# Optimization experiments

Measured on AMD Instinct MI355X. Metric: run time of the kernel, lower is better.

## Reference

```python
import jax, jax.numpy as jnp
import numpy as np

N_TOKENS = 4096
EMBED = 2048
D_ATTN = 2048


def setup_inputs() -> dict:
    key = jax.random.key(0)
    k1, k2, k3, k4 = jax.random.split(key, 4)
    # torch.rand -> uniform [0,1); keeps scores positive so the multiplicative
    # -inf mask acts as a clean causal mask (faithful to original behavior).
    token_embeddings = jax.random.uniform(k1, (N_TOKENS, EMBED), dtype=jnp.float32)
    W_Q = jax.random.uniform(k2, (EMBED, D_ATTN), dtype=jnp.float32)
    W_K = jax.random.uniform(k3, (EMBED, D_ATTN), dtype=jnp.float32)
    W_V = jax.random.uniform(k4, (EMBED, D_ATTN), dtype=jnp.float32)
    return {"token_embeddings": token_embeddings, "W_Q": W_Q, "W_K": W_K, "W_V": W_V}


def reference(token_embeddings, W_Q, W_K, W_V):
    n = token_embeddings.shape[0]
    d = W_Q.shape[1]
    # mask: 1 on/below diagonal, -inf strictly above (multiplicative, as in source)
    neg_inf = jnp.float32(-jnp.inf)
    mask = jnp.tril(jnp.ones((n, n), dtype=jnp.float32)) + jnp.triu(
        jnp.full((n, n), neg_inf, dtype=jnp.float32), k=1
    )
    Q = token_embeddings @ W_Q          # (n, d)
    K = token_embeddings @ W_K          # (n, d)
    V = token_embeddings @ W_V          # (n, d)
    scores = (Q @ K.T) * mask           # (n, n); upper tri -> -inf (scores > 0)
    scores = scores / jnp.sqrt(jnp.float32(d))
    attn = jax.nn.softmax(scores, axis=-1)
    return attn @ V                     # (n, d)
```

## Files before the change

### kernel.cpp

```cpp
#include <hip/hip_runtime.h>
#include <hip/hip_bf16.h>
#include <cstdint>
#include <cstddef>

#define N_TOK 4096
#define EMB   2048
#define DATT  2048

typedef __attribute__((ext_vector_type(8))) short short8;
typedef __attribute__((ext_vector_type(4))) short shortx4;
typedef __attribute__((ext_vector_type(4))) float f32x4;

#define MFMA(a, b, c) __builtin_amdgcn_mfma_f32_16x16x32_bf16(a, b, c, 0, 0, 0)

__device__ __forceinline__ short f2bs(float f) {
  __hip_bfloat16 h = __float2bfloat16(f);
  return __builtin_bit_cast(short, h);
}
__device__ __forceinline__ float bs2f(short s) {
  return __uint_as_float(((unsigned)(unsigned short)s) << 16);
}
__device__ __forceinline__ float ldin(const void* p, size_t i, int isbf) {
  if (isbf) {
    unsigned short u = ((const unsigned short*)p)[i];
    return __uint_as_float(((unsigned int)u) << 16);
  }
  return ((const float*)p)[i];
}

__device__ __forceinline__ size_t swz(int r, int c, int kdim) {
  return ((size_t)((r >> 7) * (kdim >> 3) + (c >> 3)) << 10) +
         (size_t)((r & 127) << 3) + (c & 7);
}

__global__ void k_sniff(const void* x, int* flag) {
  if (threadIdx.x == 0 && blockIdx.x == 0) {
    const unsigned short* u = (const unsigned short*)x;
    int bf = 1;
    for (int i = 0; i < 256; ++i) {
      unsigned short v = u[i];
      if ((v & 0x8000u) || ((v & 0x7FFFu) >= 0x3F80u)) { bf = 0; break; }
    }
    *flag = bf;
  }
}

__global__ __launch_bounds__(256) void k_xbar(const void* X, float* xbar,
                                              const int* flagp) {
  int isbf = *flagp;
  int e = blockIdx.x * 256 + threadIdx.x;
  float s = 0.f;
  for (int r = 0; r < 256; ++r) s += ldin(X, (size_t)r * EMB + e, isbf);
  xbar[e] = s * (1.f / 256.f);
}

__global__ __launch_bounds__(256) void k_split_x(const void* X, short* Xh, short* Xl,
                                                 const int* flagp) {
  int isbf = *flagp;
  size_t base = ((size_t)blockIdx.x * 256 + threadIdx.x) * 4;
  int r = (int)(base >> 11), c = (int)(base & 2047);
  shortx4 h, l;
#pragma unroll
  for (int u = 0; u < 4; ++u) {
    float x = ldin(X, base + u, isbf);
    short hh = f2bs(x);
    h[u] = hh;
    l[u] = f2bs(x - bs2f(hh));
  }
  size_t o = swz(r, c, EMB);
  *(shortx4*)(Xh + o) = h;
  *(shortx4*)(Xl + o) = l;
}

__global__ __launch_bounds__(256) void k_transpose_split(const void* W, short* Wth,
                                                         short* Wtl, int R, int C,
                                                         const int* flagp, int wlo) {
  __shared__ float T[64][65];
  int isbf = *flagp;
  int r0 = blockIdx.y * 64, c0 = blockIdx.x * 64;
  int tid = threadIdx.x;
#pragma unroll
  for (int it = 0; it < 16; ++it) {
    int idx = tid + it * 256;
    int row = idx >> 6, col = idx & 63;
    T[row][col] = ldin(W, (size_t)(r0 + row) * C + c0 + col, isbf);
  }
  __syncthreads();
#pragma unroll
  for (int it = 0; it < 16; ++it) {
    int idx = tid + it * 256;
    int row = idx >> 6, col = idx & 63;
    float x = T[col][row];
    short h = f2bs(x);
    size_t o = swz(c0 + row, r0 + col, R);
    Wth[o] = h;
    if (wlo) Wtl[o] = f2bs(x - bs2f(h));
  }
}

__global__ __launch_bounds__(256) void k_kbar(const short* Wth, const short* Wtl,
                                              const float* xbar, float* kbar) {
  int d = blockIdx.x;
  float s = 0.f;
  for (int e = threadIdx.x; e < EMB; e += 256) {
    size_t o = swz(d, e, EMB);
    s += xbar[e] * (bs2f(Wth[o]) + bs2f(Wtl[o]));
  }
  __shared__ float red[4];
#pragma unroll
  for (int off = 32; off > 0; off >>= 1) s += __shfl_down(s, off);
  if ((threadIdx.x & 63) == 0) red[threadIdx.x >> 6] = s;
  __syncthreads();
  if (threadIdx.x == 0) kbar[d] = red[0] + red[1] + red[2] + red[3];
}

__global__ __launch_bounds__(256) void k_proj_d(const short* Ah, const short* Al,
                                                const short* Bh, const short* Bl,
                                                short* Ch, short* Cl,
                                                const float* bias) {
  int tid = threadIdx.x;
  int wave = tid >> 6, lane = tid & 63;
  int ln = lane & 15, quad = lane >> 4;
  int wm = (wave >> 1) * 64, wn = (wave & 1) * 64;
  int row0 = blockIdx.y * 128, col0 = blockIdx.x * 128;
  const short8* A8h = (const short8*)Ah + (size_t)(row0 >> 7) * (256 * 128);
  const short8* A8l = (const short8*)Al + (size_t)(row0 >> 7) * (256 * 128);
  const short8* B8h = (const short8*)Bh + (size_t)(col0 >> 7) * (256 * 128);
  const short8* B8l = (const short8*)Bl + (size_t)(col0 >> 7) * (256 * 128);
  f32x4 acc[4][4] = {};
  for (int k0 = 0; k0 < EMB; k0 += 32) {
    int t = (k0 >> 3) + quad;
    short8 fah[4], fal[4], fbh[4], fbl[4];
#pragma unroll
    for (int i = 0; i < 4; ++i) {
      int ar = wm + i * 16 + ln;
      fah[i] = A8h[t * 128 + ar];
      fal[i] = A8l[t * 128 + ar];
    }
#pragma unroll
    for (int j = 0; j < 4; ++j) {
      int br = wn + j * 16 + ln;
      fbh[j] = B8h[t * 128 + br];
      fbl[j] = B8l[t * 128 + br];
    }
#pragma unroll
    for (int j = 0; j < 4; ++j)
#pragma unroll
      for (int i = 0; i < 4; ++i) {
        acc[i][j] = MFMA(fah[i], fbh[j], acc[i][j]);
        acc[i][j] = MFMA(fah[i], fbl[j], acc[i][j]);
        acc[i][j] = MFMA(fal[i], fbh[j], acc[i][j]);
      }
  }
#pragma unroll
  for (int i = 0; i < 4; ++i)
#pragma unroll
    for (int j = 0; j < 4; ++j)
#pragma unroll
      for (int r = 0; r < 4; ++r) {
        int row = row0 + wm + i * 16 + quad * 4 + r;
        int col = col0 + wn + j * 16 + ln;
        float x = acc[i][j][r];
        if (bias) x -= bias[col];
        short h = f2bs(x);
        size_t o = swz(row, col, DATT);
        Ch[o] = h;
        Cl[o] = f2bs(x - bs2f(h));
      }
}

__global__ __launch_bounds__(256) void k_proj1_d(const short* Ah, const short* Bh,
                                                 short* Ch) {
  int tid = threadIdx.x;
  int wave = tid >> 6, lane = tid & 63;
  int ln = lane & 15, quad = lane >> 4;
  int wm = (wave >> 1) * 64, wn = (wave & 1) * 64;
  int row0 = blockIdx.y * 128, col0 = blockIdx.x * 128;
  const short8* A8h = (const short8*)Ah + (size_t)(row0 >> 7) * (256 * 128);
  const short8* B8h = (const short8*)Bh + (size_t)(col0 >> 7) * (256 * 128);
  f32x4 acc[4][4] = {};
  for (int k0 = 0; k0 < EMB; k0 += 32) {
    int t = (k0 >> 3) + quad;
    short8 fah[4], fbh[4];
#pragma unroll
    for (int i = 0; i < 4; ++i) fah[i] = A8h[t * 128 + wm + i * 16 + ln];
#pragma unroll
    for (int j = 0; j < 4; ++j) fbh[j] = B8h[t * 128 + wn + j * 16 + ln];
#pragma unroll
    for (int j = 0; j < 4; ++j)
#pragma unroll
      for (int i = 0; i < 4; ++i) acc[i][j] = MFMA(fah[i], fbh[j], acc[i][j]);
  }
#pragma unroll
  for (int i = 0; i < 4; ++i)
#pragma unroll
    for (int j = 0; j < 4; ++j)
#pragma unroll
      for (int r = 0; r < 4; ++r) {
        int row = row0 + wm + i * 16 + quad * 4 + r;
        int col = col0 + wn + j * 16 + ln;
        Ch[swz(row, col, N_TOK)] = f2bs(acc[i][j][r]);
      }
}

__global__ __launch_bounds__(256) void k_score_d(const short* Qh, const short* Ql,
                                                 const short* Kh, const short* Kl,
                                                 float* S) {
  if (blockIdx.x > blockIdx.y) return;
  int tid = threadIdx.x;
  int wave = tid >> 6, lane = tid & 63;
  int ln = lane & 15, quad = lane >> 4;
  int wm = (wave >> 1) * 64, wn = (wave & 1) * 64;
  int row0 = blockIdx.y * 128, col0 = blockIdx.x * 128;
  const short8* A8h = (const short8*)Qh + (size_t)(row0 >> 7) * (256 * 128);
  const short8* A8l = (const short8*)Ql + (size_t)(row0 >> 7) * (256 * 128);
  const short8* B8h = (const short8*)Kh + (size_t)(col0 >> 7) * (256 * 128);
  const short8* B8l = (const short8*)Kl + (size_t)(col0 >> 7) * (256 * 128);
  f32x4 acc[4][4] = {};
  for (int k0 = 0; k0 < DATT; k0 += 32) {
    int t = (k0 >> 3) + quad;
    short8 fah[4], fal[4], fbh[4], fbl[4];
#pragma unroll
    for (int i = 0; i < 4; ++i) {
      int ar = wm + i * 16 + ln;
      fah[i] = A8h[t * 128 + ar];
      fal[i] = A8l[t * 128 + ar];
    }
#pragma unroll
    for (int j = 0; j < 4; ++j) {
      int br = wn + j * 16 + ln;
      fbh[j] = B8h[t * 128 + br];
      fbl[j] = B8l[t * 128 + br];
    }
#pragma unroll
    for (int j = 0; j < 4; ++j)
#pragma unroll
      for (int i = 0; i < 4; ++i) {
        acc[i][j] = MFMA(fah[i], fbh[j], acc[i][j]);
        acc[i][j] = MFMA(fah[i], fbl[j], acc[i][j]);
        acc[i][j] = MFMA(fal[i], fbh[j], acc[i][j]);
      }
  }
  const float scale = 0.022097086912079608f;
#pragma unroll
  for (int i = 0; i < 4; ++i)
#pragma unroll
    for (int j = 0; j < 4; ++j)
#pragma unroll
      for (int r = 0; r < 4; ++r) {
        int row = row0 + wm + i * 16 + quad * 4 + r;
        int col = col0 + wn + j * 16 + ln;
        if (col <= row) S[(size_t)row * N_TOK + col] = acc[i][j][r] * scale;
      }
}

__global__ __launch_bounds__(256) void k_softmax(const float* S, short* P) {
  int i = blockIdx.x;
  const float* row = S + (size_t)i * N_TOK;
  int len = i + 1;
  int tid = threadIdx.x;
  __shared__ float red[4];
  float m = -3.402823466e38f;
  for (int j = tid; j < len; j += 256) m = fmaxf(m, row[j]);
#pragma unroll
  for (int off = 32; off > 0; off >>= 1) m = fmaxf(m, __shfl_down(m, off));
  if ((tid & 63) == 0) red[tid >> 6] = m;
  __syncthreads();
  m = fmaxf(fmaxf(red[0], red[1]), fmaxf(red[2], red[3]));
  __syncthreads();
  float s = 0.f;
  for (int j = tid; j < len; j += 256) s += __expf(row[j] - m);
#pragma unroll
  for (int off = 32; off > 0; off >>= 1) s += __shfl_down(s, off);
  if ((tid & 63) == 0) red[tid >> 6] = s;
  __syncthreads();
  s = red[0] + red[1] + red[2] + red[3];
  float inv = 1.f / s;
  size_t rbase = ((size_t)(i >> 7) * (N_TOK >> 3) << 10) + (size_t)((i & 127) << 3);
  for (int j = tid; j < len; j += 256)
    P[rbase + ((size_t)(j >> 3) << 10) + (j & 7)] = f2bs(__expf(row[j] - m) * inv);
  for (int j = len + tid; j < N_TOK; j += 256)
    P[rbase + ((size_t)(j >> 3) << 10) + (j & 7)] = 0;
}

__global__ __launch_bounds__(256) void k_out_d(const short* Ph, const short* Vh,
                                               void* Co, const int* flagp) {
  int isbf = *flagp;
  int tid = threadIdx.x;
  int wave = tid >> 6, lane = tid & 63;
  int ln = lane & 15, quad = lane >> 4;
  int wm = (wave >> 1) * 64, wn = (wave & 1) * 64;
  int row0 = blockIdx.y * 128, col0 = blockIdx.x * 128;
  const short8* A8h = (const short8*)Ph + (size_t)(row0 >> 7) * (512 * 128);
  const short8* B8h = (const short8*)Vh + (size_t)(col0 >> 7) * (512 * 128);
  f32x4 acc[4][4] = {};
  int kmax = row0 + 128;
  for (int k0 = 0; k0 < kmax; k0 += 32) {
    int t = (k0 >> 3) + quad;
    short8 fah[4], fbh[4];
#pragma unroll
    for (int i = 0; i < 4; ++i) fah[i] = A8h[t * 128 + wm + i * 16 + ln];
#pragma unroll
    for (int j = 0; j < 4; ++j) fbh[j] = B8h[t * 128 + wn + j * 16 + ln];
#pragma unroll
    for (int j = 0; j < 4; ++j)
#pragma unroll
      for (int i = 0; i < 4; ++i) acc[i][j] = MFMA(fah[i], fbh[j], acc[i][j]);
  }
#pragma unroll
  for (int i = 0; i < 4; ++i)
#pragma unroll
    for (int j = 0; j < 4; ++j)
#pragma unroll
      for (int r = 0; r < 4; ++r) {
        int row = row0 + wm + i * 16 + quad * 4 + r;
        int col = col0 + wn + j * 16 + ln;
        size_t idx = (size_t)row * DATT + col;
        if (isbf) ((__hip_bfloat16*)Co)[idx] = __float2bfloat16(acc[i][j][r]);
        else      ((float*)Co)[idx] = acc[i][j][r];
      }
}

extern "C" void kernel_launch(void* const* d_in, const int* in_sizes, int n_in,
                              void* d_out, int out_size, void* d_ws, size_t ws_size,
                              hipStream_t stream) {
  const void* X  = d_in[0];
  const void* WQ = d_in[1];
  const void* WK = d_in[2];
  const void* WV = d_in[3];

  float* ws   = (float*)d_ws;
  int*   flag = (int*)d_ws;
  float* xbar = ws + 256;
  float* kbar = ws + 2560;
  short* p0   = (short*)(ws + 16384);
  const size_t M8 = (size_t)N_TOK * DATT;
  const size_t M4 = (size_t)EMB * DATT;
  short* Xh  = p0;
  short* Xl  = Xh + M8;
  short* Wth = Xl + M8;
  short* Wtl = Wth + M4;
  float* S   = (float*)p0;
  short* Qh  = p0 + 4 * M8;
  short* Ql  = Qh + M8;
  short* Kh  = Ql + M8;
  short* Kl  = Kh + M8;
  short* Vt  = Kl + M8;
  short* P   = Qh;

  dim3 blk(256);

  k_sniff<<<1, 64, 0, stream>>>(X, flag);
  k_xbar<<<EMB / 256, blk, 0, stream>>>(X, xbar, flag);
  k_split_x<<<(N_TOK * EMB) / 1024, blk, 0, stream>>>(X, Xh, Xl, flag);

  dim3 gt(DATT / 64, EMB / 64);
  dim3 gq(DATT / 128, N_TOK / 128);
  dim3 gv(N_TOK / 128, DATT / 128);

  k_transpose_split<<<gt, blk, 0, stream>>>(WQ, Wth, Wtl, EMB, DATT, flag, 1);
  k_proj_d<<<gq, blk, 0, stream>>>(Xh, Xl, Wth, Wtl, Qh, Ql, nullptr);
  k_transpose_split<<<gt, blk, 0, stream>>>(WK, Wth, Wtl, EMB, DATT, flag, 1);
  k_kbar<<<DATT, blk, 0, stream>>>(Wth, Wtl, xbar, kbar);
  k_proj_d<<<gq, blk, 0, stream>>>(Xh, Xl, Wth, Wtl, Kh, Kl, kbar);
  k_transpose_split<<<gt, blk, 0, stream>>>(WV, Wth, nullptr, EMB, DATT, flag, 0);
  k_proj1_d<<<gv, blk, 0, stream>>>(Wth, Xh, Vt);

  dim3 gs(N_TOK / 128, N_TOK / 128);
  k_score_d<<<gs, blk, 0, stream>>>(Qh, Ql, Kh, Kl, S);

  k_softmax<<<N_TOK, blk, 0, stream>>>(S, P);

  dim3 go(DATT / 128, N_TOK / 128);
  k_out_d<<<go, blk, 0, stream>>>(P, Vt, d_out, flag);
}
```

Measured before the change: 761.5 us.

## Stage GEMM tiles through double-buffered LDS via direct global-to-LDS loads

Replaces the per-wave direct global loads in all four MFMA GEMM kernels with a shared core that copies each 32-deep K chunk into LDS using global_load_lds, double-buffered so the next chunk loads while the current one is computed. The score kernel now launches only the lower-triangular tiles through a linear index decoded into (row, col) instead of a full grid with early exits. Launch bounds now request two blocks per CU. The intent is to stop each wave fetching operand tiles redundantly from global memory and to hide load latency. The cost is one barrier per K step and up to 64KB of LDS per block in the three-pass variants.

```diff
diff --git a/kernel.cpp b/kernel.cpp
--- a/kernel.cpp
+++ b/kernel.cpp
@@ -2,6 +2,7 @@
 #include <hip/hip_bf16.h>
 #include <cstdint>
 #include <cstddef>
+#include <cmath>
 
 #define N_TOK 4096
 #define EMB   2048
@@ -31,6 +32,83 @@
 __device__ __forceinline__ size_t swz(int r, int c, int kdim) {
   return ((size_t)((r >> 7) * (kdim >> 3) + (c >> 3)) << 10) +
          (size_t)((r & 127) << 3) + (c & 7);
+}
+
+__device__ __forceinline__ void gl16(const short* g, short* l) {
+  __builtin_amdgcn_global_load_lds(
+      (const __attribute__((address_space(1))) unsigned int*)(const void*)g,
+      (__attribute__((address_space(3))) unsigned int*)(void*)l, 16, 0, 0);
+}
+
+template <bool THREE>
+__device__ __forceinline__ void gemm_core(const short* Ah, const short* Al,
+                                          const short* Bh, const short* Bl,
+                                          int chunks, int apan, int bpan,
+                                          int kmax, short* lds,
+                                          f32x4 acc[4][4]) {
+  const int NSL = THREE ? 4 : 2;
+  int tid = threadIdx.x;
+  int lane = tid & 63;
+  int wave = tid >> 6;
+  int ln = lane & 15, quad = lane >> 4;
+  int wm = (wave >> 1) * 64, wn = (wave & 1) * 64;
+  int wofs = wave * 512;
+
+  auto stage = [&](int b, int k0) {
+    size_t ao = ((size_t)(apan * chunks + (k0 >> 3))) << 10;
+    size_t bo = ((size_t)(bpan * chunks + (k0 >> 3))) << 10;
+    short* base = lds + b * NSL * 4096;
+    const short* sa = Ah + ao + tid * 8;
+    const short* sb = Bh + bo + tid * 8;
+    gl16(sa,        base + wofs);
+    gl16(sa + 2048, base + wofs + 2048);
+    gl16(sb,        base + 4096 + wofs);
+    gl16(sb + 2048, base + 4096 + wofs + 2048);
+    if (THREE) {
+      const short* sal = Al + ao + tid * 8;
+      const short* sbl = Bl + bo + tid * 8;
+      gl16(sal,        base + 8192 + wofs);
+      gl16(sal + 2048, base + 8192 + wofs + 2048);
+      gl16(sbl,        base + 12288 + wofs);
+      gl16(sbl + 2048, base + 12288 + wofs + 2048);
+    }
+  };
+
+  stage(0, 0);
+  int cur = 0;
+  int abase = quad * 1024 + (wm + ln) * 8;
+  int bbase = quad * 1024 + (wn + ln) * 8;
+  for (int k0 = 0; k0 < kmax; k0 += 32) {
+    __syncthreads();
+    if (k0 + 32 < kmax) stage(cur ^ 1, k0 + 32);
+    const short* B0 = lds + cur * NSL * 4096;
+    short8 fah[4], fbh[4];
+#pragma unroll
+    for (int i = 0; i < 4; ++i) fah[i] = *(const short8*)(B0 + abase + i * 128);
+#pragma unroll
+    for (int j = 0; j < 4; ++j) fbh[j] = *(const short8*)(B0 + 4096 + bbase + j * 128);
+    if (THREE) {
+      short8 fal[4], fbl[4];
+#pragma unroll
+      for (int i = 0; i < 4; ++i) fal[i] = *(const short8*)(B0 + 8192 + abase + i * 128);
+#pragma unroll
+      for (int j = 0; j < 4; ++j) fbl[j] = *(const short8*)(B0 + 12288 + bbase + j * 128);
+#pragma unroll
+      for (int j = 0; j < 4; ++j)
+#pragma unroll
+        for (int i = 0; i < 4; ++i) {
+          acc[i][j] = MFMA(fah[i], fbh[j], acc[i][j]);
+          acc[i][j] = MFMA(fah[i], fbl[j], acc[i][j]);
+          acc[i][j] = MFMA(fal[i], fbh[j], acc[i][j]);
+        }
+    } else {
+#pragma unroll
+      for (int j = 0; j < 4; ++j)
+#pragma unroll
+        for (int i = 0; i < 4; ++i) acc[i][j] = MFMA(fah[i], fbh[j], acc[i][j]);
+    }
+    cur ^= 1;
+  }
 }
 
 __global__ void k_sniff(const void* x, int* flag) {
@@ -114,44 +192,18 @@
   if (threadIdx.x == 0) kbar[d] = red[0] + red[1] + red[2] + red[3];
 }
 
-__global__ __launch_bounds__(256) void k_proj_d(const short* Ah, const short* Al,
-                                                const short* Bh, const short* Bl,
-                                                short* Ch, short* Cl,
-                                                const float* bias) {
+__global__ __launch_bounds__(256, 2) void k_proj3(const short* Ah, const short* Al,
+                                                  const short* Bh, const short* Bl,
+                                                  short* Ch, short* Cl,
+                                                  const float* bias) {
+  __shared__ short lds[2 * 4 * 4096];
+  f32x4 acc[4][4] = {};
+  int row0 = blockIdx.y * 128, col0 = blockIdx.x * 128;
+  gemm_core<true>(Ah, Al, Bh, Bl, EMB >> 3, row0 >> 7, col0 >> 7, EMB, lds, acc);
   int tid = threadIdx.x;
   int wave = tid >> 6, lane = tid & 63;
   int ln = lane & 15, quad = lane >> 4;
   int wm = (wave >> 1) * 64, wn = (wave & 1) * 64;
-  int row0 = blockIdx.y * 128, col0 = blockIdx.x * 128;
-  const short8* A8h = (const short8*)Ah + (size_t)(row0 >> 7) * (256 * 128);
-  const short8* A8l = (const short8*)Al + (size_t)(row0 >> 7) * (256 * 128);
-  const short8* B8h = (const short8*)Bh + (size_t)(col0 >> 7) * (256 * 128);
-  const short8* B8l = (const short8*)Bl + (size_t)(col0 >> 7) * (256 * 128);
-  f32x4 acc[4][4] = {};
-  for (int k0 = 0; k0 < EMB; k0 += 32) {
-    int t = (k0 >> 3) + quad;
-    short8 fah[4], fal[4], fbh[4], fbl[4];
-#pragma unroll
-    for (int i = 0; i < 4; ++i) {
-      int ar = wm + i * 16 + ln;
-      fah[i] = A8h[t * 128 + ar];
-      fal[i] = A8l[t * 128 + ar];
-    }
-#pragma unroll
-    for (int j = 0; j < 4; ++j) {
-      int br = wn + j * 16 + ln;
-      fbh[j] = B8h[t * 128 + br];
-      fbl[j] = B8l[t * 128 + br];
-    }
-#pragma unroll
-    for (int j = 0; j < 4; ++j)
-#pragma unroll
-      for (int i = 0; i < 4; ++i) {
-        acc[i][j] = MFMA(fah[i], fbh[j], acc[i][j]);
-        acc[i][j] = MFMA(fah[i], fbl[j], acc[i][j]);
-        acc[i][j] = MFMA(fal[i], fbh[j], acc[i][j]);
-      }
-  }
 #pragma unroll
   for (int i = 0; i < 4; ++i)
 #pragma unroll
@@ -169,28 +221,17 @@
       }
 }
 
-__global__ __launch_bounds__(256) void k_proj1_d(const short* Ah, const short* Bh,
-                                                 short* Ch) {
+__global__ __launch_bounds__(256, 2) void k_proj1(const short* Ah, const short* Bh,
+                                                  short* Ch) {
+  __shared__ short lds[2 * 2 * 4096];
+  f32x4 acc[4][4] = {};
+  int row0 = blockIdx.y * 128, col0 = blockIdx.x * 128;
+  gemm_core<false>(Ah, nullptr, Bh, nullptr, EMB >> 3, row0 >> 7, col0 >> 7, EMB,
+                   lds, acc);
   int tid = threadIdx.x;
   int wave = tid >> 6, lane = tid & 63;
   int ln = lane & 15, quad = lane >> 4;
   int wm = (wave >> 1) * 64, wn = (wave & 1) * 64;
-  int row0 = blockIdx.y * 128, col0 = blockIdx.x * 128;
-  const short8* A8h = (const short8*)Ah + (size_t)(row0 >> 7) * (256 * 128);
-  const short8* B8h = (const short8*)Bh + (size_t)(col0 >> 7) * (256 * 128);
-  f32x4 acc[4][4] = {};
-  for (int k0 = 0; k0 < EMB; k0 += 32) {
-    int t = (k0 >> 3) + quad;
-    short8 fah[4], fbh[4];
-#pragma unroll
-    for (int i = 0; i < 4; ++i) fah[i] = A8h[t * 128 + wm + i * 16 + ln];
-#pragma unroll
-    for (int j = 0; j < 4; ++j) fbh[j] = B8h[t * 128 + wn + j * 16 + ln];
-#pragma unroll
-    for (int j = 0; j < 4; ++j)
-#pragma unroll
-      for (int i = 0; i < 4; ++i) acc[i][j] = MFMA(fah[i], fbh[j], acc[i][j]);
-  }
 #pragma unroll
   for (int i = 0; i < 4; ++i)
 #pragma unroll
@@ -203,44 +244,22 @@
       }
 }
 
-__global__ __launch_bounds__(256) void k_score_d(const short* Qh, const short* Ql,
-                                                 const short* Kh, const short* Kl,
-                                                 float* S) {
-  if (blockIdx.x > blockIdx.y) return;
+__global__ __launch_bounds__(256, 2) void k_score3(const short* Qh, const short* Ql,
+                                                   const short* Kh, const short* Kl,
+                                                   float* S) {
+  int bi = blockIdx.x;
+  int by = (int)((sqrtf(8.f * (float)bi + 1.f) - 1.f) * 0.5f);
+  while ((by + 1) * (by + 2) / 2 <= bi) ++by;
+  while (by * (by + 1) / 2 > bi) --by;
+  int bx = bi - by * (by + 1) / 2;
+  __shared__ short lds[2 * 4 * 4096];
+  f32x4 acc[4][4] = {};
+  gemm_core<true>(Qh, Ql, Kh, Kl, DATT >> 3, by, bx, DATT, lds, acc);
+  int row0 = by * 128, col0 = bx * 128;
   int tid = threadIdx.x;
   int wave = tid >> 6, lane = tid & 63;
   int ln = lane & 15, quad = lane >> 4;
   int wm = (wave >> 1) * 64, wn = (wave & 1) * 64;
-  int row0 = blockIdx.y * 128, col0 = blockIdx.x * 128;
-  const short8* A8h = (const short8*)Qh + (size_t)(row0 >> 7) * (256 * 128);
-  const short8* A8l = (const short8*)Ql + (size_t)(row0 >> 7) * (256 * 128);
-  const short8* B8h = (const short8*)Kh + (size_t)(col0 >> 7) * (256 * 128);
-  const short8* B8l = (const short8*)Kl + (size_t)(col0 >> 7) * (256 * 128);
-  f32x4 acc[4][4] = {};
-  for (int k0 = 0; k0 < DATT; k0 += 32) {
-    int t = (k0 >> 3) + quad;
-    short8 fah[4], fal[4], fbh[4], fbl[4];
-#pragma unroll
-    for (int i = 0; i < 4; ++i) {
-      int ar = wm + i * 16 + ln;
-      fah[i] = A8h[t * 128 + ar];
-      fal[i] = A8l[t * 128 + ar];
-    }
-#pragma unroll
-    for (int j = 0; j < 4; ++j) {
-      int br = wn + j * 16 + ln;
-      fbh[j] = B8h[t * 128 + br];
-      fbl[j] = B8l[t * 128 + br];
-    }
-#pragma unroll
-    for (int j = 0; j < 4; ++j)
-#pragma unroll
-      for (int i = 0; i < 4; ++i) {
-        acc[i][j] = MFMA(fah[i], fbh[j], acc[i][j]);
-        acc[i][j] = MFMA(fah[i], fbl[j], acc[i][j]);
-        acc[i][j] = MFMA(fal[i], fbh[j], acc[i][j]);
-      }
-  }
   const float scale = 0.022097086912079608f;
 #pragma unroll
   for (int i = 0; i < 4; ++i)
@@ -283,30 +302,18 @@
     P[rbase + ((size_t)(j >> 3) << 10) + (j & 7)] = 0;
 }
 
-__global__ __launch_bounds__(256) void k_out_d(const short* Ph, const short* Vh,
-                                               void* Co, const int* flagp) {
+__global__ __launch_bounds__(256, 2) void k_out(const short* Ph, const short* Vh,
+                                                void* Co, const int* flagp) {
+  __shared__ short lds[2 * 2 * 4096];
+  f32x4 acc[4][4] = {};
+  int row0 = blockIdx.y * 128, col0 = blockIdx.x * 128;
+  gemm_core<false>(Ph, nullptr, Vh, nullptr, N_TOK >> 3, row0 >> 7, col0 >> 7,
+                   row0 + 128, lds, acc);
   int isbf = *flagp;
   int tid = threadIdx.x;
   int wave = tid >> 6, lane = tid & 63;
   int ln = lane & 15, quad = lane >> 4;
   int wm = (wave >> 1) * 64, wn = (wave & 1) * 64;
-  int row0 = blockIdx.y * 128, col0 = blockIdx.x * 128;
-  const short8* A8h = (const short8*)Ph + (size_t)(row0 >> 7) * (512 * 128);
-  const short8* B8h = (const short8*)Vh + (size_t)(col0 >> 7) * (512 * 128);
-  f32x4 acc[4][4] = {};
-  int kmax = row0 + 128;
-  for (int k0 = 0; k0 < kmax; k0 += 32) {
-    int t = (k0 >> 3) + quad;
-    short8 fah[4], fbh[4];
-#pragma unroll
-    for (int i = 0; i < 4; ++i) fah[i] = A8h[t * 128 + wm + i * 16 + ln];
-#pragma unroll
-    for (int j = 0; j < 4; ++j) fbh[j] = B8h[t * 128 + wn + j * 16 + ln];
-#pragma unroll
-    for (int j = 0; j < 4; ++j)
-#pragma unroll
-      for (int i = 0; i < 4; ++i) acc[i][j] = MFMA(fah[i], fbh[j], acc[i][j]);
-  }
 #pragma unroll
   for (int i = 0; i < 4; ++i)
 #pragma unroll
@@ -359,18 +366,18 @@
   dim3 gv(N_TOK / 128, DATT / 128);
 
   k_transpose_split<<<gt, blk, 0, stream>>>(WQ, Wth, Wtl, EMB, DATT, flag, 1);
-  k_proj_d<<<gq, blk, 0, stream>>>(Xh, Xl, Wth, Wtl, Qh, Ql, nullptr);
+  k_proj3<<<gq, blk, 0, stream>>>(Xh, Xl, Wth, Wtl, Qh, Ql, nullptr);
   k_transpose_split<<<gt, blk, 0, stream>>>(WK, Wth, Wtl, EMB, DATT, flag, 1);
   k_kbar<<<DATT, blk, 0, stream>>>(Wth, Wtl, xbar, kbar);
-  k_proj_d<<<gq, blk, 0, stream>>>(Xh, Xl, Wth, Wtl, Kh, Kl, kbar);
+  k_proj3<<<gq, blk, 0, stream>>>(Xh, Xl, Wth, Wtl, Kh, Kl, kbar);
   k_transpose_split<<<gt, blk, 0, stream>>>(WV, Wth, nullptr, EMB, DATT, flag, 0);
-  k_proj1_d<<<gv, blk, 0, stream>>>(Wth, Xh, Vt);
-
-  dim3 gs(N_TOK / 128, N_TOK / 128);
-  k_score_d<<<gs, blk, 0, stream>>>(Qh, Ql, Kh, Kl, S);
+  k_proj1<<<gv, blk, 0, stream>>>(Wth, Xh, Vt);
+
+  dim3 gs((N_TOK / 128) * (N_TOK / 128 + 1) / 2);
+  k_score3<<<gs, blk, 0, stream>>>(Qh, Ql, Kh, Kl, S);
 
   k_softmax<<<N_TOK, blk, 0, stream>>>(S, P);
 
   dim3 go(DATT / 128, N_TOK / 128);
-  k_out_d<<<go, blk, 0, stream>>>(P, Vt, d_out, flag);
-}
+  k_out<<<go, blk, 0, stream>>>(P, Vt, d_out, flag);
+}
```

New measurement: 700.1 us. 8.1% less time.
